# Kernel optimization log

Measured on AMD Instinct MI355X. Metric: run time of the kernel, lower is better.

The kernel has to match this reference:

```python
import jax, jax.numpy as jnp
import numpy as np

SIZE = 7  # spatial size, matches init kwarg


def setup_inputs() -> dict:
    key = jax.random.key(0)
    k1, k2 = jax.random.split(key, 2)
    N, C, H, W = 256, 2048, SIZE, SIZE
    x = jax.random.normal(k1, (N, C, H, W), dtype=jnp.float32)
    # nn.Linear(2*C, 2): weight (2, 2C), bias (2,)
    Wlin = jax.random.normal(k2, (2, 2 * C), dtype=jnp.float32) * 0.02
    b = jnp.zeros((2,), dtype=jnp.float32)
    return {"x": x, "Wlin": Wlin, "b": b}


def reference(x, Wlin, b):
    N, C, H, W = x.shape
    HW = H * W
    size = SIZE
    # (N, HW, C) token view
    rx = x.reshape(N, C, HW).transpose(0, 2, 1)
    # index of max mean-activation token per sample
    idx = jnp.argmax(jnp.mean(rx, axis=-1), axis=-1)  # (N,)
    bidx = jnp.arange(N)
    max_feat = rx[bidx, idx]  # (N, C)
    # concat(max_feat, rx) @ Wlin.T + b, split to avoid materializing (N,HW,2C)
    W1, W2 = Wlin[:, :C], Wlin[:, C:]
    pred = jax.nn.relu(
        jnp.einsum('npc,oc->npo', rx, W2) + (max_feat @ W1.T)[:, None, :] + b
    )  # (N, HW, 2)
    # zero out prediction at the anchor token
    pred = pred.at[bidx, idx].set(0.0)
    # basic label grid (i, j)
    ii, jj = jnp.meshgrid(jnp.arange(H), jnp.arange(W), indexing='ij')
    label = jnp.stack([ii, jj], axis=-1).reshape(HW, 2).astype(x.dtype)  # (HW, 2)
    anchor = label[idx][:, None, :]  # (N, 1, 2)
    rel = (label[None, :, :] - anchor) / size  # (N, HW, 2)
    rel_dist = jnp.sqrt(jnp.sum(rel ** 2, axis=-1))  # (N, HW)
    rel_angle = (jnp.arctan2(rel[..., 1], rel[..., 0]) / jnp.pi + 1) / 2  # (N, HW)
    dist_loss = (pred[..., 0] - rel_dist) ** 2
    gap = pred[..., 1] - rel_angle
    gap = jnp.where(gap < 0, gap + 1, gap)
    gap = gap - jnp.mean(gap, axis=-1, keepdims=True)
    return (dist_loss + gap ** 2).reshape(N, H, W)
```

## Files before the change

### kernel.cpp

```cpp
#include <hip/hip_runtime.h>
#include <hip/hip_bf16.h>
#include <math.h>

#define N_BATCH 256
#define C_CH    2048
#define HW      49
#define SIZE7   7
#define BLOCK   1024
#define WAVES   16
#define C_PER_W (C_CH / WAVES)

__global__ __launch_bounds__(BLOCK) void rpp_fused_kernel(
    const float* __restrict__ x, const float* __restrict__ Wlin,
    const float* __restrict__ b, float* __restrict__ out) {
  const int n    = blockIdx.x;
  const int tid  = threadIdx.x;
  const int lane = tid & 63;
  const int wave = tid >> 6;

  __shared__ __align__(16) float wlin_s[2 * 2 * C_CH];
  __shared__ float red[WAVES][5][64];

  {
    const float4* src = (const float4*)Wlin;
    float4* dst = (float4*)wlin_s;
#pragma unroll
    for (int i = tid; i < 2 * C_CH; i += BLOCK) dst[i] = src[i];
  }
  __syncthreads();

  const float* w1r0 = wlin_s;
  const float* w1r1 = wlin_s + 4096;
  const float* w2r0 = wlin_s + 2048;
  const float* w2r1 = wlin_s + 6144;

  const int lp = (lane < HW) ? lane : 0;
  const int cbase = wave * C_PER_W;
  const float* xp = x + (size_t)n * C_CH * HW + (size_t)cbase * HW + lp;

  float a0 = 0.f, a1 = 0.f, a2 = 0.f, a3 = 0.f, a4 = 0.f;
#pragma unroll 4
  for (int c = 0; c < C_PER_W; c += 4, xp += 4 * HW) {
    const float v0 = xp[0 * HW];
    const float v1 = xp[1 * HW];
    const float v2 = xp[2 * HW];
    const float v3 = xp[3 * HW];
    const float4 w0 = *(const float4*)&w1r0[cbase + c];
    const float4 w1 = *(const float4*)&w1r1[cbase + c];
    const float4 w2 = *(const float4*)&w2r0[cbase + c];
    const float4 w3 = *(const float4*)&w2r1[cbase + c];
    a0 += (v0 + v1) + (v2 + v3);
    a1 = fmaf(v0, w0.x, fmaf(v1, w0.y, fmaf(v2, w0.z, fmaf(v3, w0.w, a1))));
    a2 = fmaf(v0, w1.x, fmaf(v1, w1.y, fmaf(v2, w1.z, fmaf(v3, w1.w, a2))));
    a3 = fmaf(v0, w2.x, fmaf(v1, w2.y, fmaf(v2, w2.z, fmaf(v3, w2.w, a3))));
    a4 = fmaf(v0, w3.x, fmaf(v1, w3.y, fmaf(v2, w3.z, fmaf(v3, w3.w, a4))));
  }

  red[wave][0][lane] = a0;
  red[wave][1][lane] = a1;
  red[wave][2][lane] = a2;
  red[wave][3][lane] = a3;
  red[wave][4][lane] = a4;
  __syncthreads();

  if (wave != 0) return;

  float s0 = 0.f, s1 = 0.f, s2 = 0.f, s3 = 0.f, s4 = 0.f;
#pragma unroll
  for (int w = 0; w < WAVES; w++) {
    s0 += red[w][0][lane];
    s1 += red[w][1][lane];
    s2 += red[w][2][lane];
    s3 += red[w][3][lane];
    s4 += red[w][4][lane];
  }

  float v = (lane < HW) ? s0 : -INFINITY;
  int vi = lane;
#pragma unroll
  for (int off = 32; off; off >>= 1) {
    const float ov = __shfl_down(v, off);
    const int oi = __shfl_down(vi, off);
    if (ov > v || (ov == v && oi < vi)) { v = ov; vi = oi; }
  }
  const int idx = __shfl(vi, 0);

  const float anc0 = __shfl(s1, idx);
  const float anc1 = __shfl(s2, idx);
  const float b0 = b[0], b1 = b[1];

  float pred0 = fmaxf(s3 + anc0 + b0, 0.f);
  float pred1 = fmaxf(s4 + anc1 + b1, 0.f);
  if (lane == idx) { pred0 = 0.f; pred1 = 0.f; }

  const int li = lane / SIZE7, lj = lane % SIZE7;
  const int ai = idx / SIZE7, aj = idx % SIZE7;
  const float ri = (float)(li - ai) * (1.0f / SIZE7);
  const float rj = (float)(lj - aj) * (1.0f / SIZE7);
  const float rdist = sqrtf(ri * ri + rj * rj);
  const float rangle = atan2f(rj, ri) * 0.15915494309189535f + 0.5f;

  float dl = pred0 - rdist;
  dl *= dl;
  float gap = pred1 - rangle;
  if (gap < 0.f) gap += 1.f;

  float g = (lane < HW) ? gap : 0.f;
#pragma unroll
  for (int off = 32; off; off >>= 1) g += __shfl_down(g, off);
  const float mean = __shfl(g, 0) * (1.0f / HW);
  gap -= mean;

  if (lane < HW) out[(size_t)n * HW + lane] = dl + gap * gap;
}

extern "C" void kernel_launch(void* const* d_in, const int* in_sizes, int n_in,
                              void* d_out, int out_size, void* d_ws, size_t ws_size,
                              hipStream_t stream) {
  const float* x    = (const float*)d_in[0];
  const float* Wlin = (const float*)d_in[1];
  const float* b    = (const float*)d_in[2];
  float* out = (float*)d_out;
  (void)d_ws; (void)ws_size;

  hipLaunchKernelGGL(rpp_fused_kernel, dim3(N_BATCH), dim3(BLOCK), 0,
                     stream, x, Wlin, b, out);
}
```

Before: 155.8 us.

## Load x as float4 over 4-channel groups with per-element weight select

The loop now treats each group of 4 channels (196 contiguous floats) as 49 float4 loads, one per lane, instead of scalar loads at stride 49. Each lane works out which channel each of its four elements belongs to and selects the matching weight. Partial sums are reduced across waves and across the four sub-positions through a larger shared buffer. This is meant to cut the number of load instructions and raise memory efficiency, at the cost of extra select logic, more shared memory and an extra reduction stage.

```diff
diff --git a/kernel.cpp b/kernel.cpp
--- a/kernel.cpp
+++ b/kernel.cpp
@@ -8,9 +8,9 @@
 #define SIZE7   7
 #define BLOCK   1024
 #define WAVES   16
-#define C_PER_W (C_CH / WAVES)
+#define GRP_PER_W 32
 
-__global__ __launch_bounds__(BLOCK) void rpp_fused_kernel(
+__global__ __launch_bounds__(BLOCK) void rpp_fused2_kernel(
     const float* __restrict__ x, const float* __restrict__ Wlin,
     const float* __restrict__ b, float* __restrict__ out) {
   const int n    = blockIdx.x;
@@ -18,62 +18,87 @@
   const int lane = tid & 63;
   const int wave = tid >> 6;
 
-  __shared__ __align__(16) float wlin_s[2 * 2 * C_CH];
-  __shared__ float red[WAVES][5][64];
+  __shared__ __align__(16) float w_s[4][C_CH];
+  __shared__ __align__(16) float red2[WAVES][5][64][4];
+  __shared__ float sfin[5][HW];
 
   {
     const float4* src = (const float4*)Wlin;
-    float4* dst = (float4*)wlin_s;
-#pragma unroll
-    for (int i = tid; i < 2 * C_CH; i += BLOCK) dst[i] = src[i];
+    float4* dst = (float4*)w_s;
+    for (int j = tid; j < 2048; j += BLOCK) {
+      const int q = j >> 9, c4 = j & 511;
+      dst[j] = src[(q & 1) * 1024 + (q >> 1) * 512 + c4];
+    }
   }
   __syncthreads();
 
-  const float* w1r0 = wlin_s;
-  const float* w1r1 = wlin_s + 4096;
-  const float* w2r0 = wlin_s + 2048;
-  const float* w2r1 = wlin_s + 6144;
-
-  const int lp = (lane < HW) ? lane : 0;
-  const int cbase = wave * C_PER_W;
-  const float* xp = x + (size_t)n * C_CH * HW + (size_t)cbase * HW + lp;
-
-  float a0 = 0.f, a1 = 0.f, a2 = 0.f, a3 = 0.f, a4 = 0.f;
-#pragma unroll 4
-  for (int c = 0; c < C_PER_W; c += 4, xp += 4 * HW) {
-    const float v0 = xp[0 * HW];
-    const float v1 = xp[1 * HW];
-    const float v2 = xp[2 * HW];
-    const float v3 = xp[3 * HW];
-    const float4 w0 = *(const float4*)&w1r0[cbase + c];
-    const float4 w1 = *(const float4*)&w1r1[cbase + c];
-    const float4 w2 = *(const float4*)&w2r0[cbase + c];
-    const float4 w3 = *(const float4*)&w2r1[cbase + c];
-    a0 += (v0 + v1) + (v2 + v3);
-    a1 = fmaf(v0, w0.x, fmaf(v1, w0.y, fmaf(v2, w0.z, fmaf(v3, w0.w, a1))));
-    a2 = fmaf(v0, w1.x, fmaf(v1, w1.y, fmaf(v2, w1.z, fmaf(v3, w1.w, a2))));
-    a3 = fmaf(v0, w2.x, fmaf(v1, w2.y, fmaf(v2, w2.z, fmaf(v3, w2.w, a3))));
-    a4 = fmaf(v0, w3.x, fmaf(v1, w3.y, fmaf(v2, w3.z, fmaf(v3, w3.w, a4))));
+  const int l = (lane < HW) ? lane : 0;
+  int cm[4];
+#pragma unroll
+  for (int m = 0; m < 4; m++) {
+    const int e = 4 * l + m;
+    cm[m] = (e >= 49) + (e >= 98) + (e >= 147);
   }
 
-  red[wave][0][lane] = a0;
-  red[wave][1][lane] = a1;
-  red[wave][2][lane] = a2;
-  red[wave][3][lane] = a3;
-  red[wave][4][lane] = a4;
+  const float* xg = x + (size_t)n * (C_CH * HW)
+                      + (size_t)wave * (GRP_PER_W * 196) + 4 * l;
+
+  float acc[5][4];
+#pragma unroll
+  for (int q = 0; q < 5; q++)
+#pragma unroll
+    for (int m = 0; m < 4; m++) acc[q][m] = 0.f;
+
+  int gg = wave * GRP_PER_W;
+#pragma unroll 4
+  for (int i = 0; i < GRP_PER_W; i++, gg++, xg += 196) {
+    const float4 v = *(const float4*)xg;
+    const float4 u0 = *(const float4*)&w_s[0][4 * gg];
+    const float4 u1 = *(const float4*)&w_s[1][4 * gg];
+    const float4 u2 = *(const float4*)&w_s[2][4 * gg];
+    const float4 u3 = *(const float4*)&w_s[3][4 * gg];
+    const float xv[4] = {v.x, v.y, v.z, v.w};
+#pragma unroll
+    for (int m = 0; m < 4; m++) {
+      const int c = cm[m];
+      const float w0 = (c == 0) ? u0.x : (c == 1) ? u0.y : (c == 2) ? u0.z : u0.w;
+      const float w1 = (c == 0) ? u1.x : (c == 1) ? u1.y : (c == 2) ? u1.z : u1.w;
+      const float w2 = (c == 0) ? u2.x : (c == 1) ? u2.y : (c == 2) ? u2.z : u2.w;
+      const float w3 = (c == 0) ? u3.x : (c == 1) ? u3.y : (c == 2) ? u3.z : u3.w;
+      acc[0][m] += xv[m];
+      acc[1][m] = fmaf(xv[m], w0, acc[1][m]);
+      acc[2][m] = fmaf(xv[m], w1, acc[2][m]);
+      acc[3][m] = fmaf(xv[m], w2, acc[3][m]);
+      acc[4][m] = fmaf(xv[m], w3, acc[4][m]);
+    }
+  }
+
+#pragma unroll
+  for (int q = 0; q < 5; q++) {
+    const float4 t = make_float4(acc[q][0], acc[q][1], acc[q][2], acc[q][3]);
+    *(float4*)&red2[wave][q][lane][0] = t;
+  }
+  __syncthreads();
+
+  if (tid < 5 * HW) {
+    const int q = tid / HW, p = tid % HW;
+    float s = 0.f;
+#pragma unroll
+    for (int w = 0; w < WAVES; w++)
+#pragma unroll
+      for (int k = 0; k < 4; k++) {
+        const int e = p + 49 * k;
+        s += red2[w][q][e >> 2][e & 3];
+      }
+    sfin[q][p] = s;
+  }
   __syncthreads();
 
   if (wave != 0) return;
 
-  float s0 = 0.f, s1 = 0.f, s2 = 0.f, s3 = 0.f, s4 = 0.f;
-#pragma unroll
-  for (int w = 0; w < WAVES; w++) {
-    s0 += red[w][0][lane];
-    s1 += red[w][1][lane];
-    s2 += red[w][2][lane];
-    s3 += red[w][3][lane];
-    s4 += red[w][4][lane];
-  }
+  const int pl = (lane < HW) ? lane : 0;
+  const float s0 = sfin[0][pl], s1 = sfin[1][pl], s2 = sfin[2][pl];
+  const float s3 = sfin[3][pl], s4 = sfin[4][pl];
 
   float v = (lane < HW) ? s0 : -INFINITY;
   int vi = lane;
@@ -123,6 +148,6 @@
   float* out = (float*)d_out;
   (void)d_ws; (void)ws_size;
 
-  hipLaunchKernelGGL(rpp_fused_kernel, dim3(N_BATCH), dim3(BLOCK), 0,
+  hipLaunchKernelGGL(rpp_fused2_kernel, dim3(N_BATCH), dim3(BLOCK), 0,
                      stream, x, Wlin, b, out);
 }
```

After: 155.0 us. No clear change (-0.5%).
